# Performance work log

Measured on AMD Instinct MI355X. Metric: run time of the kernel, lower is better.

## Reference

```python
import jax, jax.numpy as jnp
import numpy as np

B, P, ED, AD, DD, E, V, T = 64, 196, 2048, 512, 512, 300, 1000, 96


def setup_inputs() -> dict:
    key = jax.random.key(0)
    ks = jax.random.split(key, 24)
    s = 0.02  # small init scale for weights
    lens = jax.random.randint(ks[2], (B,), 2, T + 1).astype(jnp.int32)
    lens = lens.at[0].set(T)  # ensure max(decode_lengths) == T-1 (static)
    return {
        'encoder_out': jax.random.normal(ks[0], (B, P, ED), jnp.float32),
        'encoded_captions': jax.random.randint(ks[1], (B, T), 0, V),
        'caption_lengths': lens,
        'emb': jax.random.uniform(ks[3], (V, E), jnp.float32, -0.1, 0.1),
        'W_enc_att': jax.random.normal(ks[4], (ED, AD), jnp.float32) * s,
        'b_enc_att': jnp.zeros((AD,), jnp.float32),
        'W_dec_att': jax.random.normal(ks[5], (DD, AD), jnp.float32) * s,
        'b_dec_att': jnp.zeros((AD,), jnp.float32),
        'w_full': jax.random.normal(ks[6], (AD,), jnp.float32) * s,
        'b_full': jnp.zeros((), jnp.float32),
        'W_init_h': jax.random.normal(ks[7], (ED, DD), jnp.float32) * s,
        'b_init_h': jnp.zeros((DD,), jnp.float32),
        'W_init_c': jax.random.normal(ks[8], (ED, DD), jnp.float32) * s,
        'b_init_c': jnp.zeros((DD,), jnp.float32),
        'W_fbeta': jax.random.normal(ks[9], (DD, ED), jnp.float32) * s,
        'b_fbeta': jnp.zeros((ED,), jnp.float32),
        'W_ih': jax.random.normal(ks[10], (E + ED, 4 * DD), jnp.float32) * s,
        'b_ih': jnp.zeros((4 * DD,), jnp.float32),
        'W_hh': jax.random.normal(ks[11], (DD, 4 * DD), jnp.float32) * s,
        'b_hh': jnp.zeros((4 * DD,), jnp.float32),
        'W_fc': jax.random.uniform(ks[12], (DD, V), jnp.float32, -0.1, 0.1),
        'b_fc': jnp.zeros((V,), jnp.float32),
    }


def reference(encoder_out, encoded_captions, caption_lengths, emb,
              W_enc_att, b_enc_att, W_dec_att, b_dec_att, w_full, b_full,
              W_init_h, b_init_h, W_init_c, b_init_c, W_fbeta, b_fbeta,
              W_ih, b_ih, W_hh, b_hh, W_fc, b_fc):
    # Sort by caption length, descending (stable like torch.sort on ints)
    sort_ind = jnp.argsort(-caption_lengths)
    lens = caption_lengths[sort_ind]
    eo = encoder_out[sort_ind]                  # [B,P,ED]
    caps = encoded_captions[sort_ind]           # [B,T]
    decode_lengths = lens - 1                   # [B]

    embs = emb[caps]                            # [B,T,E]
    mean_eo = eo.mean(axis=1)                   # [B,ED]
    h0 = mean_eo @ W_init_h + b_init_h          # [B,DD]
    c0 = mean_eo @ W_init_c + b_init_c

    # encoder-side attention projection is step-invariant: hoist it
    att1 = eo @ W_enc_att + b_enc_att           # [B,P,AD]

    Tdec = T - 1
    ts = jnp.arange(Tdec)
    masks = (decode_lengths[None, :] > ts[:, None]).astype(eo.dtype)  # [Tdec,B]
    emb_seq = jnp.swapaxes(embs[:, :Tdec, :], 0, 1)                    # [Tdec,B,E]

    def step(carry, xs):
        h, c = carry
        emb_t, m = xs                           # [B,E], [B]
        mb = m[:, None]
        # Bahdanau attention
        att2 = h @ W_dec_att + b_dec_att        # [B,AD]
        e = jnp.einsum('bpa,a->bp', jax.nn.relu(att1 + att2[:, None, :]), w_full) + b_full
        alpha = jax.nn.softmax(e, axis=1)       # [B,P]
        awe = jnp.einsum('bpd,bp->bd', eo, alpha)  # [B,ED]
        gate = jax.nn.sigmoid(h @ W_fbeta + b_fbeta)
        x = jnp.concatenate([emb_t, gate * awe], axis=1)  # [B,E+ED]
        # LSTMCell (torch gate order: i, f, g, o)
        gates = x @ W_ih + b_ih + h @ W_hh + b_hh
        i, f, g, o = jnp.split(gates, 4, axis=1)
        c_new = jax.nn.sigmoid(f) * c + jax.nn.sigmoid(i) * jnp.tanh(g)
        h_new = jax.nn.sigmoid(o) * jnp.tanh(c_new)
        # only active rows (sorted so they are a prefix) update state
        h2 = mb * h_new + (1.0 - mb) * h
        c2 = mb * c_new + (1.0 - mb) * c
        preds = (h2 @ W_fc + b_fc) * mb         # dropout = identity (eval)
        return (h2, c2), (preds, alpha * mb)

    (_, _), (preds, alphas) = jax.lax.scan(step, (h0, c0), (emb_seq, masks))
    predictions = jnp.swapaxes(preds, 0, 1)     # [B,Tdec,V]
    alphas = jnp.swapaxes(alphas, 0, 1)         # [B,Tdec,P]
    return predictions, caps, decode_lengths, alphas, sort_ind
```

## Files before the change

kernel.cpp:

```cpp
#include <hip/hip_runtime.h>
#include <stddef.h>
#include <math.h>

static constexpr int B = 64, P = 196, ED = 2048, AD = 512, DD = 512, E = 300, V = 1000, T = 96, TD = 95;
static constexpr int KX = E + ED;
static constexpr int KTOT = KX + DD;
static constexpr int KSPLIT = 8;
static constexpr int KPER = 368;
static constexpr int NG = 4 * DD;

static constexpr size_t POFF   = 0;
static constexpr size_t CAPOFF = (size_t)B * TD * V;
static constexpr size_t DLOFF  = CAPOFF + (size_t)B * T;
static constexpr size_t AOFF   = DLOFF + B;
static constexpr size_t SOFF   = AOFF + (size_t)B * TD * P;

__device__ __forceinline__ float sigm(float x) { return 1.0f / (1.0f + expf(-x)); }

__global__ __launch_bounds__(64) void k_sort(const int* __restrict__ lens,
                                             const int* __restrict__ caps_in,
                                             int* __restrict__ sidx,
                                             int* __restrict__ dlen,
                                             int* __restrict__ caps_s,
                                             float* __restrict__ out) {
    __shared__ int sl[B];
    __shared__ int ss[B];
    int i = threadIdx.x;
    sl[i] = lens[i];
    __syncthreads();
    int li = sl[i];
    int r = 0;
    for (int j = 0; j < B; j++) {
        int lj = sl[j];
        r += (lj > li) || (lj == li && j < i);
    }
    ss[r] = i;
    sidx[r] = i;
    dlen[r] = li - 1;
    out[DLOFF + r] = (float)(li - 1);
    out[SOFF + r] = (float)i;
    __syncthreads();
    for (int idx = i; idx < B * T; idx += B) {
        int b = idx / T, tt = idx % T;
        int v = caps_in[ss[b] * T + tt];
        caps_s[idx] = v;
        out[CAPOFF + idx] = (float)v;
    }
}

__global__ __launch_bounds__(256) void k_mean(const float* __restrict__ eo,
                                              const int* __restrict__ sidx,
                                              float* __restrict__ mean_eo) {
    int b = blockIdx.y;
    int d = blockIdx.x * 256 + threadIdx.x;
    const float* base = eo + ((size_t)sidx[b] * P) * ED + d;
    float s = 0.f;
    for (int p = 0; p < P; p++) s += base[(size_t)p * ED];
    mean_eo[(size_t)b * ED + d] = s * (1.0f / (float)P);
}

__global__ __launch_bounds__(256) void k_init(const float* __restrict__ mean_eo,
                                              const float* __restrict__ Wh, const float* __restrict__ bh,
                                              const float* __restrict__ Wc, const float* __restrict__ bc,
                                              float* __restrict__ h0, float* __restrict__ c0,
                                              float* __restrict__ xT) {
    int idx = blockIdx.x * 256 + threadIdx.x;
    int b = idx >> 9, j = idx & 511;
    const float* m = mean_eo + (size_t)b * ED;
    float ah = bh[j], ac = bc[j];
    for (int k = 0; k < ED; k++) {
        float mv = m[k];
        ah += mv * Wh[(size_t)k * DD + j];
        ac += mv * Wc[(size_t)k * DD + j];
    }
    h0[idx] = ah;
    c0[idx] = ac;
    xT[(size_t)(KX + j) * B + b] = ah;
}

__global__ __launch_bounds__(256) void k_att1(const float* __restrict__ eo,
                                              const float* __restrict__ W,
                                              const float* __restrict__ bias,
                                              const int* __restrict__ sidx,
                                              float* __restrict__ att1) {
    int m0 = blockIdx.x * 64, n0 = blockIdx.y * 64;
    __shared__ float sA[16][68];
    __shared__ float sB[16][68];
    int tid = threadIdx.x;
    int tx = tid & 15, ty = tid >> 4;
    float acc[4][4] = {};

    int la_m = tid >> 2;
    int la_k = (tid & 3) * 4;
    int lb_k = tid >> 4;
    int lb_n = (tid & 15) * 4;

    int mA = m0 + la_m;
    int bA = mA / P, pA = mA % P;
    const float* arow = eo + ((size_t)sidx[bA] * P + pA) * ED;

    for (int k0 = 0; k0 < ED; k0 += 16) {
        float4 av = *(const float4*)(arow + k0 + la_k);
        sA[la_k + 0][la_m] = av.x;
        sA[la_k + 1][la_m] = av.y;
        sA[la_k + 2][la_m] = av.z;
        sA[la_k + 3][la_m] = av.w;
        float4 bv = *(const float4*)(W + (size_t)(k0 + lb_k) * AD + n0 + lb_n);
        *(float4*)&sB[lb_k][lb_n] = bv;
        __syncthreads();
#pragma unroll
        for (int kk = 0; kk < 16; kk++) {
            float4 a4 = *(const float4*)&sA[kk][ty * 4];
            float4 b4 = *(const float4*)&sB[kk][tx * 4];
            float av_[4] = {a4.x, a4.y, a4.z, a4.w};
            float bv_[4] = {b4.x, b4.y, b4.z, b4.w};
#pragma unroll
            for (int i = 0; i < 4; i++)
#pragma unroll
                for (int j = 0; j < 4; j++) acc[i][j] += av_[i] * bv_[j];
        }
        __syncthreads();
    }
#pragma unroll
    for (int i = 0; i < 4; i++) {
        int m = m0 + ty * 4 + i;
        int n = n0 + tx * 4;
        float4 o;
        o.x = acc[i][0] + bias[n + 0];
        o.y = acc[i][1] + bias[n + 1];
        o.z = acc[i][2] + bias[n + 2];
        o.w = acc[i][3] + bias[n + 3];
        *(float4*)(att1 + (size_t)m * AD + n) = o;
    }
}

__global__ __launch_bounds__(256) void kA1(const float* __restrict__ hprev,
                                           const float* __restrict__ Wda, const float* __restrict__ bda,
                                           const float* __restrict__ Wfb, const float* __restrict__ bfb,
                                           const float* __restrict__ emb,
                                           const int* __restrict__ caps_s,
                                           float* __restrict__ att2g,
                                           float* __restrict__ fg,
                                           float* __restrict__ xT, int t) {
    int bx = blockIdx.x;
    int tid = threadIdx.x;
    if (bx >= 80) {
        int k0 = (bx - 80) * 60;
        for (int l = tid; l < 60 * 64; l += 256) {
            int r = l >> 6, b = l & 63;
            int k = k0 + r;
            int cap = caps_s[b * T + t];
            xT[(size_t)k * B + b] = emb[(size_t)cap * E + k];
        }
        return;
    }
    int n0 = bx * 32;
    bool is_att = (n0 < AD);
    __shared__ float sH[16][68];
    __shared__ float sW[16][36];
    float acc[4][2] = {};
    int tb = tid & 15, tn = tid >> 4;

    for (int k0 = 0; k0 < DD; k0 += 16) {
        {
            int b = tid >> 2, q = tid & 3;
            float4 hv = *(const float4*)(hprev + (size_t)b * DD + k0 + q * 4);
            sH[q * 4 + 0][b] = hv.x;
            sH[q * 4 + 1][b] = hv.y;
            sH[q * 4 + 2][b] = hv.z;
            sH[q * 4 + 3][b] = hv.w;
        }
        if (tid < 128) {
            int kk = tid >> 3, nn = (tid & 7) * 4;
            float4 wv;
            if (is_att) wv = *(const float4*)(Wda + (size_t)(k0 + kk) * AD + n0 + nn);
            else        wv = *(const float4*)(Wfb + (size_t)(k0 + kk) * ED + (n0 - AD) + nn);
            *(float4*)&sW[kk][nn] = wv;
        }
        __syncthreads();
#pragma unroll
        for (int kk = 0; kk < 16; kk++) {
            float4 hv = *(const float4*)&sH[kk][tb * 4];
            float w0 = sW[kk][tn * 2 + 0];
            float w1 = sW[kk][tn * 2 + 1];
            acc[0][0] += hv.x * w0; acc[0][1] += hv.x * w1;
            acc[1][0] += hv.y * w0; acc[1][1] += hv.y * w1;
            acc[2][0] += hv.z * w0; acc[2][1] += hv.z * w1;
            acc[3][0] += hv.w * w0; acc[3][1] += hv.w * w1;
        }
        __syncthreads();
    }
#pragma unroll
    for (int i = 0; i < 4; i++)
#pragma unroll
        for (int j = 0; j < 2; j++) {
            int b = tb * 4 + i;
            int n = n0 + tn * 2 + j;
            float v = acc[i][j];
            if (is_att) att2g[(size_t)b * AD + n] = v + bda[n];
            else {
                int d = n - AD;
                fg[(size_t)b * ED + d] = sigm(v + bfb[d]);
            }
        }
}

__global__ __launch_bounds__(256) void kA2(const float* __restrict__ att2g,
                                           const float* __restrict__ att1,
                                           const float* __restrict__ wf,
                                           const float* __restrict__ bfv,
                                           const int* __restrict__ dlen,
                                           float* __restrict__ alpha,
                                           float* __restrict__ out, int t) {
    int b = blockIdx.x;
    int tid = threadIdx.x;
    __shared__ float sa2[AD];
    __shared__ float swf[AD];
    __shared__ float se[P];
    __shared__ float red[256];

    sa2[tid] = att2g[(size_t)b * AD + tid];
    sa2[tid + 256] = att2g[(size_t)b * AD + tid + 256];
    swf[tid] = wf[tid];
    swf[tid + 256] = wf[tid + 256];
    __syncthreads();

    int w = tid >> 6, lane = tid & 63;
    float bf0 = bfv[0];
    for (int p = w; p < P; p += 4) {
        const float* row = att1 + ((size_t)b * P + p) * AD + lane * 8;
        float4 u0 = *(const float4*)row;
        float4 u1 = *(const float4*)(row + 4);
        float4 s0 = *(const float4*)&sa2[lane * 8];
        float4 s1 = *(const float4*)&sa2[lane * 8 + 4];
        float4 w0 = *(const float4*)&swf[lane * 8];
        float4 w1 = *(const float4*)&swf[lane * 8 + 4];
        float acc = fmaxf(u0.x + s0.x, 0.f) * w0.x + fmaxf(u0.y + s0.y, 0.f) * w0.y +
                    fmaxf(u0.z + s0.z, 0.f) * w0.z + fmaxf(u0.w + s0.w, 0.f) * w0.w +
                    fmaxf(u1.x + s1.x, 0.f) * w1.x + fmaxf(u1.y + s1.y, 0.f) * w1.y +
                    fmaxf(u1.z + s1.z, 0.f) * w1.z + fmaxf(u1.w + s1.w, 0.f) * w1.w;
#pragma unroll
        for (int m = 32; m >= 1; m >>= 1) acc += __shfl_xor(acc, m, 64);
        if (lane == 0) se[p] = acc + bf0;
    }
    __syncthreads();

    red[tid] = (tid < P) ? se[tid] : -1e30f;
    __syncthreads();
    for (int s = 128; s > 0; s >>= 1) {
        if (tid < s) red[tid] = fmaxf(red[tid], red[tid + s]);
        __syncthreads();
    }
    float mx = red[0];
    __syncthreads();
    float ex = (tid < P) ? expf(se[tid] - mx) : 0.f;
    red[tid] = ex;
    __syncthreads();
    for (int s = 128; s > 0; s >>= 1) {
        if (tid < s) red[tid] += red[tid + s];
        __syncthreads();
    }
    float inv = 1.0f / red[0];
    if (tid < P) {
        float a = ex * inv;
        alpha[(size_t)b * P + tid] = a;
        float m = (dlen[b] > t) ? 1.f : 0.f;
        out[AOFF + ((size_t)b * TD + t) * P + tid] = a * m;
    }
}

__global__ __launch_bounds__(256) void kB(const float* __restrict__ eo,
                                          const int* __restrict__ sidx,
                                          const float* __restrict__ alpha,
                                          const float* __restrict__ fg,
                                          float* __restrict__ xT) {
    int b = blockIdx.y, ch = blockIdx.x, tid = threadIdx.x;
    __shared__ float sal[P];
    if (tid < P) sal[tid] = alpha[(size_t)b * P + tid];
    __syncthreads();
    int d = ch * 256 + tid;
    const float* base = eo + ((size_t)sidx[b] * P) * ED + d;
    float aw = 0.f;
    for (int p = 0; p < P; p++) aw += base[(size_t)p * ED] * sal[p];
    xT[(size_t)(E + d) * B + b] = fg[(size_t)b * ED + d] * aw;
}

__global__ __launch_bounds__(256) void kC(const float* __restrict__ xT,
                                          const float* __restrict__ Wih,
                                          const float* __restrict__ Whh,
                                          float* __restrict__ part) {
    int bx = blockIdx.x;
    int ks = bx >> 6, nb = bx & 63;
    int n0 = nb * 32;
    int tid = threadIdx.x;
    int tb = tid & 15, tn = tid >> 4;
    __shared__ float sW[16][36];
    float acc[4][2] = {};
    int kbase = ks * KPER;

    for (int tile = 0; tile < 23; tile++) {
        int k0 = kbase + tile * 16;
        if (tid < 128) {
            int kk = tid >> 3, nn = (tid & 7) * 4;
            int kg = k0 + kk;
            float4 wv = make_float4(0.f, 0.f, 0.f, 0.f);
            if (kg < KX) wv = *(const float4*)&Wih[(size_t)kg * NG + n0 + nn];
            else if (kg < KTOT) wv = *(const float4*)&Whh[(size_t)(kg - KX) * NG + n0 + nn];
            *(float4*)&sW[kk][nn] = wv;
        }
        __syncthreads();
#pragma unroll
        for (int kk = 0; kk < 16; kk++) {
            int kg = k0 + kk;
            float4 xv = make_float4(0.f, 0.f, 0.f, 0.f);
            if (kg < KTOT) xv = *(const float4*)&xT[(size_t)kg * B + tb * 4];
            float w0 = sW[kk][tn * 2 + 0];
            float w1 = sW[kk][tn * 2 + 1];
            acc[0][0] += xv.x * w0; acc[0][1] += xv.x * w1;
            acc[1][0] += xv.y * w0; acc[1][1] += xv.y * w1;
            acc[2][0] += xv.z * w0; acc[2][1] += xv.z * w1;
            acc[3][0] += xv.w * w0; acc[3][1] += xv.w * w1;
        }
        __syncthreads();
    }
    float* pr = part + (size_t)ks * B * NG;
#pragma unroll
    for (int i = 0; i < 4; i++)
#pragma unroll
        for (int j = 0; j < 2; j++) {
            int b = tb * 4 + i, n = n0 + tn * 2 + j;
            pr[(size_t)b * NG + n] = acc[i][j];
        }
}

__global__ __launch_bounds__(256) void kD(const float* __restrict__ part,
                                          const float* __restrict__ bih,
                                          const float* __restrict__ bhh,
                                          const float* __restrict__ hprev,
                                          const float* __restrict__ cc,
                                          const int* __restrict__ dlen,
                                          float* __restrict__ hseq_t,
                                          float* __restrict__ cn,
                                          float* __restrict__ xT, int t) {
    int idx = blockIdx.x * 256 + threadIdx.x;
    int b = idx >> 9, j = idx & 511;
    float gi = bih[j] + bhh[j];
    float gf = bih[DD + j] + bhh[DD + j];
    float gg = bih[2 * DD + j] + bhh[2 * DD + j];
    float go = bih[3 * DD + j] + bhh[3 * DD + j];
#pragma unroll
    for (int s = 0; s < KSPLIT; s++) {
        const float* pr = part + ((size_t)s * B + b) * NG;
        gi += pr[j];
        gf += pr[DD + j];
        gg += pr[2 * DD + j];
        go += pr[3 * DD + j];
    }
    float cold = cc[idx], hold = hprev[idx];
    float cnew = sigm(gf) * cold + sigm(gi) * tanhf(gg);
    float hnew = sigm(go) * tanhf(cnew);
    bool m = dlen[b] > t;
    float h2 = m ? hnew : hold;
    float c2 = m ? cnew : cold;
    hseq_t[idx] = h2;
    cn[idx] = c2;
    xT[(size_t)(KX + j) * B + b] = h2;
}

__global__ __launch_bounds__(256) void k_predsall(const float* __restrict__ hseq,
                                                  const float* __restrict__ Wfc,
                                                  const float* __restrict__ bfc,
                                                  const int* __restrict__ dlen,
                                                  float* __restrict__ out) {
    int t = blockIdx.x;
    int n0 = blockIdx.y * 64;
    int tid = threadIdx.x;
    int tx = tid & 15, ty = tid >> 4;
    __shared__ float sA[16][68];
    __shared__ float sB[16][68];
    float acc[4][4] = {};
    const float* A = hseq + (size_t)t * B * DD;

    for (int k0 = 0; k0 < DD; k0 += 16) {
        {
            int b = tid >> 2, q = tid & 3;
            float4 hv = *(const float4*)(A + (size_t)b * DD + k0 + q * 4);
            sA[q * 4 + 0][b] = hv.x;
            sA[q * 4 + 1][b] = hv.y;
            sA[q * 4 + 2][b] = hv.z;
            sA[q * 4 + 3][b] = hv.w;
        }
        {
            int kk = tid >> 4, nn = (tid & 15) * 4;
            int c = n0 + nn;
            const float* wrow = Wfc + (size_t)(k0 + kk) * V;
            float4 wv;
            if (c + 3 < V) wv = *(const float4*)(wrow + c);
            else {
                wv.x = (c + 0 < V) ? wrow[c + 0] : 0.f;
                wv.y = (c + 1 < V) ? wrow[c + 1] : 0.f;
                wv.z = (c + 2 < V) ? wrow[c + 2] : 0.f;
                wv.w = (c + 3 < V) ? wrow[c + 3] : 0.f;
            }
            *(float4*)&sB[kk][nn] = wv;
        }
        __syncthreads();
#pragma unroll
        for (int kk = 0; kk < 16; kk++) {
            float4 a4 = *(const float4*)&sA[kk][ty * 4];
            float4 b4 = *(const float4*)&sB[kk][tx * 4];
            float av_[4] = {a4.x, a4.y, a4.z, a4.w};
            float bv_[4] = {b4.x, b4.y, b4.z, b4.w};
#pragma unroll
            for (int i = 0; i < 4; i++)
#pragma unroll
                for (int j = 0; j < 4; j++) acc[i][j] += av_[i] * bv_[j];
        }
        __syncthreads();
    }
#pragma unroll
    for (int i = 0; i < 4; i++) {
        int b = ty * 4 + i;
        bool m = dlen[b] > t;
#pragma unroll
        for (int j = 0; j < 4; j++) {
            int n = n0 + tx * 4 + j;
            if (n < V)
                out[POFF + ((size_t)b * TD + t) * V + n] = m ? (acc[i][j] + bfc[n]) : 0.f;
        }
    }
}

extern "C" void kernel_launch(void* const* d_in, const int* in_sizes, int n_in,
                              void* d_out, int out_size, void* d_ws, size_t ws_size,
                              hipStream_t stream) {
    const float* eo    = (const float*)d_in[0];
    const int*   caps  = (const int*)d_in[1];
    const int*   lens  = (const int*)d_in[2];
    const float* emb   = (const float*)d_in[3];
    const float* Wea   = (const float*)d_in[4];
    const float* bea   = (const float*)d_in[5];
    const float* Wda   = (const float*)d_in[6];
    const float* bda   = (const float*)d_in[7];
    const float* wfull = (const float*)d_in[8];
    const float* bfull = (const float*)d_in[9];
    const float* Wih_  = (const float*)d_in[10];
    const float* bih_  = (const float*)d_in[11];
    const float* Wic   = (const float*)d_in[12];
    const float* bic   = (const float*)d_in[13];
    const float* Wfb   = (const float*)d_in[14];
    const float* bfb   = (const float*)d_in[15];
    const float* Wih   = (const float*)d_in[16];
    const float* bih   = (const float*)d_in[17];
    const float* Whh   = (const float*)d_in[18];
    const float* bhh   = (const float*)d_in[19];
    const float* Wfc   = (const float*)d_in[20];
    const float* bfc   = (const float*)d_in[21];
    float* out = (float*)d_out;

    char* w = (char*)d_ws;
    auto carve = [&](size_t bytes) -> void* {
        void* p = (void*)w;
        w += (bytes + 255) & ~(size_t)255;
        return p;
    };
    int* sidx      = (int*)carve(B * 4);
    int* dlen      = (int*)carve(B * 4);
    int* caps_s    = (int*)carve((size_t)B * T * 4);
    float* mean_eo = (float*)carve((size_t)B * ED * 4);
    float* h0      = (float*)carve((size_t)B * DD * 4);
    float* cb0     = (float*)carve((size_t)B * DD * 4);
    float* cb1     = (float*)carve((size_t)B * DD * 4);
    float* att1    = (float*)carve((size_t)B * P * AD * 4);
    float* alphaW  = (float*)carve((size_t)B * P * 4);
    float* att2g   = (float*)carve((size_t)B * AD * 4);
    float* fg      = (float*)carve((size_t)B * ED * 4);
    float* xT      = (float*)carve((size_t)KTOT * B * 4);
    float* part    = (float*)carve((size_t)KSPLIT * B * NG * 4);
    float* hseq    = (float*)carve((size_t)TD * B * DD * 4);
    float* cb[2] = {cb0, cb1};

    k_sort<<<1, 64, 0, stream>>>(lens, caps, sidx, dlen, caps_s, out);
    k_mean<<<dim3(ED / 256, B), 256, 0, stream>>>(eo, sidx, mean_eo);
    k_init<<<(B * DD) / 256, 256, 0, stream>>>(mean_eo, Wih_, bih_, Wic, bic, h0, cb0, xT);
    k_att1<<<dim3((B * P) / 64, AD / 64), 256, 0, stream>>>(eo, Wea, bea, sidx, att1);

    for (int t = 0; t < TD; t++) {
        const float* hprev = (t == 0) ? h0 : (hseq + (size_t)(t - 1) * B * DD);
        float* cc = cb[t & 1];
        float* cn = cb[(t + 1) & 1];
        kA1<<<85, 256, 0, stream>>>(hprev, Wda, bda, Wfb, bfb, emb, caps_s, att2g, fg, xT, t);
        kA2<<<64, 256, 0, stream>>>(att2g, att1, wfull, bfull, dlen, alphaW, out, t);
        kB<<<dim3(8, B), 256, 0, stream>>>(eo, sidx, alphaW, fg, xT);
        kC<<<512, 256, 0, stream>>>(xT, Wih, Whh, part);
        kD<<<(B * DD) / 256, 256, 0, stream>>>(part, bih, bhh, hprev, cc, dlen,
                                               hseq + (size_t)t * B * DD, cn, xT, t);
    }
    k_predsall<<<dim3(TD, 16), 256, 0, stream>>>(hseq, Wfc, bfc, dlen, out);
}
```

Baseline: 19.51 ms.

## Fuse per-timestep decoder kernels into one persistent cooperative kernel with grid syncs

Replaces the five kernels launched per timestep with a single cooperative kernel (256 blocks of 512 threads) that loops over all timesteps and separates the phases with grid.sync(). This removes about 475 kernel launches and their gaps. The LSTM gate GEMM is also restructured: K-split is cut from 8 to 4, there is no shared-memory tiling, and each thread reads weights directly per column. In exchange, grid-wide barriers replace kernel boundaries, and the simpler GEMM may use bandwidth less efficiently.

```diff
diff --git a/kernel.cpp b/kernel.cpp
--- a/kernel.cpp
+++ b/kernel.cpp
@@ -1,12 +1,15 @@
 #include <hip/hip_runtime.h>
+#include <hip/hip_cooperative_groups.h>
 #include <stddef.h>
 #include <math.h>
+
+namespace cg = cooperative_groups;
 
 static constexpr int B = 64, P = 196, ED = 2048, AD = 512, DD = 512, E = 300, V = 1000, T = 96, TD = 95;
 static constexpr int KX = E + ED;
 static constexpr int KTOT = KX + DD;
-static constexpr int KSPLIT = 8;
-static constexpr int KPER = 368;
+static constexpr int NS = 4;
+static constexpr int KPER2 = KTOT / NS;
 static constexpr int NG = 4 * DD;
 
 static constexpr size_t POFF   = 0;
@@ -134,237 +137,209 @@
     }
 }
 
-__global__ __launch_bounds__(256) void kA1(const float* __restrict__ hprev,
-                                           const float* __restrict__ Wda, const float* __restrict__ bda,
-                                           const float* __restrict__ Wfb, const float* __restrict__ bfb,
-                                           const float* __restrict__ emb,
-                                           const int* __restrict__ caps_s,
-                                           float* __restrict__ att2g,
-                                           float* __restrict__ fg,
-                                           float* __restrict__ xT, int t) {
-    int bx = blockIdx.x;
-    int tid = threadIdx.x;
-    if (bx >= 80) {
-        int k0 = (bx - 80) * 60;
-        for (int l = tid; l < 60 * 64; l += 256) {
-            int r = l >> 6, b = l & 63;
-            int k = k0 + r;
-            int cap = caps_s[b * T + t];
-            xT[(size_t)k * B + b] = emb[(size_t)cap * E + k];
-        }
-        return;
-    }
-    int n0 = bx * 32;
-    bool is_att = (n0 < AD);
+__global__ __launch_bounds__(512, 2) void k_steps(
+    const float* __restrict__ eo, const int* __restrict__ sidx,
+    const int* __restrict__ dlen, const int* __restrict__ caps_s,
+    const float* __restrict__ emb,
+    const float* __restrict__ Wda, const float* __restrict__ bda,
+    const float* __restrict__ Wfb, const float* __restrict__ bfb,
+    const float* __restrict__ wfull, const float* __restrict__ bfull,
+    const float* __restrict__ att1,
+    const float* __restrict__ Wih, const float* __restrict__ Whh,
+    const float* __restrict__ bih, const float* __restrict__ bhh,
+    const float* __restrict__ h0, float* __restrict__ cb0, float* __restrict__ cb1,
+    float* __restrict__ att2g, float* __restrict__ fg, float* __restrict__ xT,
+    float* __restrict__ part, float* __restrict__ alphaW,
+    float* __restrict__ hseq, float* __restrict__ out)
+{
+    cg::grid_group grid = cg::this_grid();
+    const int bid = blockIdx.x;
+    const int tid = threadIdx.x;
+
     __shared__ float sH[16][68];
     __shared__ float sW[16][36];
-    float acc[4][2] = {};
-    int tb = tid & 15, tn = tid >> 4;
-
-    for (int k0 = 0; k0 < DD; k0 += 16) {
-        {
-            int b = tid >> 2, q = tid & 3;
-            float4 hv = *(const float4*)(hprev + (size_t)b * DD + k0 + q * 4);
-            sH[q * 4 + 0][b] = hv.x;
-            sH[q * 4 + 1][b] = hv.y;
-            sH[q * 4 + 2][b] = hv.z;
-            sH[q * 4 + 3][b] = hv.w;
-        }
-        if (tid < 128) {
-            int kk = tid >> 3, nn = (tid & 7) * 4;
-            float4 wv;
-            if (is_att) wv = *(const float4*)(Wda + (size_t)(k0 + kk) * AD + n0 + nn);
-            else        wv = *(const float4*)(Wfb + (size_t)(k0 + kk) * ED + (n0 - AD) + nn);
-            *(float4*)&sW[kk][nn] = wv;
-        }
-        __syncthreads();
-#pragma unroll
-        for (int kk = 0; kk < 16; kk++) {
-            float4 hv = *(const float4*)&sH[kk][tb * 4];
-            float w0 = sW[kk][tn * 2 + 0];
-            float w1 = sW[kk][tn * 2 + 1];
-            acc[0][0] += hv.x * w0; acc[0][1] += hv.x * w1;
-            acc[1][0] += hv.y * w0; acc[1][1] += hv.y * w1;
-            acc[2][0] += hv.z * w0; acc[2][1] += hv.z * w1;
-            acc[3][0] += hv.w * w0; acc[3][1] += hv.w * w1;
-        }
-        __syncthreads();
-    }
-#pragma unroll
-    for (int i = 0; i < 4; i++)
-#pragma unroll
-        for (int j = 0; j < 2; j++) {
-            int b = tb * 4 + i;
-            int n = n0 + tn * 2 + j;
-            float v = acc[i][j];
-            if (is_att) att2g[(size_t)b * AD + n] = v + bda[n];
-            else {
-                int d = n - AD;
-                fg[(size_t)b * ED + d] = sigm(v + bfb[d]);
-            }
-        }
-}
-
-__global__ __launch_bounds__(256) void kA2(const float* __restrict__ att2g,
-                                           const float* __restrict__ att1,
-                                           const float* __restrict__ wf,
-                                           const float* __restrict__ bfv,
-                                           const int* __restrict__ dlen,
-                                           float* __restrict__ alpha,
-                                           float* __restrict__ out, int t) {
-    int b = blockIdx.x;
-    int tid = threadIdx.x;
     __shared__ float sa2[AD];
     __shared__ float swf[AD];
     __shared__ float se[P];
-    __shared__ float red[256];
-
-    sa2[tid] = att2g[(size_t)b * AD + tid];
-    sa2[tid + 256] = att2g[(size_t)b * AD + tid + 256];
-    swf[tid] = wf[tid];
-    swf[tid + 256] = wf[tid + 256];
-    __syncthreads();
-
-    int w = tid >> 6, lane = tid & 63;
-    float bf0 = bfv[0];
-    for (int p = w; p < P; p += 4) {
-        const float* row = att1 + ((size_t)b * P + p) * AD + lane * 8;
-        float4 u0 = *(const float4*)row;
-        float4 u1 = *(const float4*)(row + 4);
-        float4 s0 = *(const float4*)&sa2[lane * 8];
-        float4 s1 = *(const float4*)&sa2[lane * 8 + 4];
-        float4 w0 = *(const float4*)&swf[lane * 8];
-        float4 w1 = *(const float4*)&swf[lane * 8 + 4];
-        float acc = fmaxf(u0.x + s0.x, 0.f) * w0.x + fmaxf(u0.y + s0.y, 0.f) * w0.y +
-                    fmaxf(u0.z + s0.z, 0.f) * w0.z + fmaxf(u0.w + s0.w, 0.f) * w0.w +
-                    fmaxf(u1.x + s1.x, 0.f) * w1.x + fmaxf(u1.y + s1.y, 0.f) * w1.y +
-                    fmaxf(u1.z + s1.z, 0.f) * w1.z + fmaxf(u1.w + s1.w, 0.f) * w1.w;
-#pragma unroll
-        for (int m = 32; m >= 1; m >>= 1) acc += __shfl_xor(acc, m, 64);
-        if (lane == 0) se[p] = acc + bf0;
-    }
-    __syncthreads();
-
-    red[tid] = (tid < P) ? se[tid] : -1e30f;
-    __syncthreads();
-    for (int s = 128; s > 0; s >>= 1) {
-        if (tid < s) red[tid] = fmaxf(red[tid], red[tid + s]);
-        __syncthreads();
-    }
-    float mx = red[0];
-    __syncthreads();
-    float ex = (tid < P) ? expf(se[tid] - mx) : 0.f;
-    red[tid] = ex;
-    __syncthreads();
-    for (int s = 128; s > 0; s >>= 1) {
-        if (tid < s) red[tid] += red[tid + s];
-        __syncthreads();
-    }
-    float inv = 1.0f / red[0];
-    if (tid < P) {
-        float a = ex * inv;
-        alpha[(size_t)b * P + tid] = a;
-        float m = (dlen[b] > t) ? 1.f : 0.f;
-        out[AOFF + ((size_t)b * TD + t) * P + tid] = a * m;
-    }
-}
-
-__global__ __launch_bounds__(256) void kB(const float* __restrict__ eo,
-                                          const int* __restrict__ sidx,
-                                          const float* __restrict__ alpha,
-                                          const float* __restrict__ fg,
-                                          float* __restrict__ xT) {
-    int b = blockIdx.y, ch = blockIdx.x, tid = threadIdx.x;
+    __shared__ float red[512];
     __shared__ float sal[P];
-    if (tid < P) sal[tid] = alpha[(size_t)b * P + tid];
-    __syncthreads();
-    int d = ch * 256 + tid;
-    const float* base = eo + ((size_t)sidx[b] * P) * ED + d;
-    float aw = 0.f;
-    for (int p = 0; p < P; p++) aw += base[(size_t)p * ED] * sal[p];
-    xT[(size_t)(E + d) * B + b] = fg[(size_t)b * ED + d] * aw;
-}
-
-__global__ __launch_bounds__(256) void kC(const float* __restrict__ xT,
-                                          const float* __restrict__ Wih,
-                                          const float* __restrict__ Whh,
-                                          float* __restrict__ part) {
-    int bx = blockIdx.x;
-    int ks = bx >> 6, nb = bx & 63;
-    int n0 = nb * 32;
-    int tid = threadIdx.x;
-    int tb = tid & 15, tn = tid >> 4;
-    __shared__ float sW[16][36];
-    float acc[4][2] = {};
-    int kbase = ks * KPER;
-
-    for (int tile = 0; tile < 23; tile++) {
-        int k0 = kbase + tile * 16;
-        if (tid < 128) {
-            int kk = tid >> 3, nn = (tid & 7) * 4;
-            int kg = k0 + kk;
-            float4 wv = make_float4(0.f, 0.f, 0.f, 0.f);
-            if (kg < KX) wv = *(const float4*)&Wih[(size_t)kg * NG + n0 + nn];
-            else if (kg < KTOT) wv = *(const float4*)&Whh[(size_t)(kg - KX) * NG + n0 + nn];
-            *(float4*)&sW[kk][nn] = wv;
-        }
-        __syncthreads();
-#pragma unroll
-        for (int kk = 0; kk < 16; kk++) {
-            int kg = k0 + kk;
-            float4 xv = make_float4(0.f, 0.f, 0.f, 0.f);
-            if (kg < KTOT) xv = *(const float4*)&xT[(size_t)kg * B + tb * 4];
-            float w0 = sW[kk][tn * 2 + 0];
-            float w1 = sW[kk][tn * 2 + 1];
-            acc[0][0] += xv.x * w0; acc[0][1] += xv.x * w1;
-            acc[1][0] += xv.y * w0; acc[1][1] += xv.y * w1;
-            acc[2][0] += xv.z * w0; acc[2][1] += xv.z * w1;
-            acc[3][0] += xv.w * w0; acc[3][1] += xv.w * w1;
-        }
-        __syncthreads();
-    }
-    float* pr = part + (size_t)ks * B * NG;
-#pragma unroll
-    for (int i = 0; i < 4; i++)
-#pragma unroll
-        for (int j = 0; j < 2; j++) {
-            int b = tb * 4 + i, n = n0 + tn * 2 + j;
-            pr[(size_t)b * NG + n] = acc[i][j];
-        }
-}
-
-__global__ __launch_bounds__(256) void kD(const float* __restrict__ part,
-                                          const float* __restrict__ bih,
-                                          const float* __restrict__ bhh,
-                                          const float* __restrict__ hprev,
-                                          const float* __restrict__ cc,
-                                          const int* __restrict__ dlen,
-                                          float* __restrict__ hseq_t,
-                                          float* __restrict__ cn,
-                                          float* __restrict__ xT, int t) {
-    int idx = blockIdx.x * 256 + threadIdx.x;
-    int b = idx >> 9, j = idx & 511;
-    float gi = bih[j] + bhh[j];
-    float gf = bih[DD + j] + bhh[DD + j];
-    float gg = bih[2 * DD + j] + bhh[2 * DD + j];
-    float go = bih[3 * DD + j] + bhh[3 * DD + j];
-#pragma unroll
-    for (int s = 0; s < KSPLIT; s++) {
-        const float* pr = part + ((size_t)s * B + b) * NG;
-        gi += pr[j];
-        gf += pr[DD + j];
-        gg += pr[2 * DD + j];
-        go += pr[3 * DD + j];
-    }
-    float cold = cc[idx], hold = hprev[idx];
-    float cnew = sigm(gf) * cold + sigm(gi) * tanhf(gg);
-    float hnew = sigm(go) * tanhf(cnew);
-    bool m = dlen[b] > t;
-    float h2 = m ? hnew : hold;
-    float c2 = m ? cnew : cold;
-    hseq_t[idx] = h2;
-    cn[idx] = c2;
-    xT[(size_t)(KX + j) * B + b] = h2;
+
+#pragma unroll 1
+    for (int t = 0; t < TD; t++) {
+        const float* hprev = (t == 0) ? h0 : (hseq + (size_t)(t - 1) * B * DD);
+
+        if (bid < 80) {
+            int n0 = bid * 32;
+            bool is_att = (n0 < AD);
+            const float* W = is_att ? Wda : Wfb;
+            int ld = is_att ? AD : ED;
+            int colb = is_att ? n0 : (n0 - AD);
+            int tb = tid & 15, tn = tid >> 4;
+            float a0 = 0.f, a1 = 0.f, a2 = 0.f, a3 = 0.f;
+            for (int k0 = 0; k0 < DD; k0 += 16) {
+                if (tid < 256) {
+                    int b = tid >> 2, q = tid & 3;
+                    float4 hv = *(const float4*)(hprev + (size_t)b * DD + k0 + q * 4);
+                    sH[q * 4 + 0][b] = hv.x;
+                    sH[q * 4 + 1][b] = hv.y;
+                    sH[q * 4 + 2][b] = hv.z;
+                    sH[q * 4 + 3][b] = hv.w;
+                }
+                if (tid < 128) {
+                    int kk = tid >> 3, nn = (tid & 7) * 4;
+                    *(float4*)&sW[kk][nn] = *(const float4*)(W + (size_t)(k0 + kk) * ld + colb + nn);
+                }
+                __syncthreads();
+#pragma unroll
+                for (int kk = 0; kk < 16; kk++) {
+                    float4 hv = *(const float4*)&sH[kk][tb * 4];
+                    float wv = sW[kk][tn];
+                    a0 += hv.x * wv; a1 += hv.y * wv; a2 += hv.z * wv; a3 += hv.w * wv;
+                }
+                __syncthreads();
+            }
+            float accv[4] = {a0, a1, a2, a3};
+            int n = n0 + tn;
+            if (is_att) {
+                float bv = bda[n];
+#pragma unroll
+                for (int i = 0; i < 4; i++)
+                    att2g[(size_t)(tb * 4 + i) * AD + n] = accv[i] + bv;
+            } else {
+                int d = n - AD;
+                float bv = bfb[d];
+#pragma unroll
+                for (int i = 0; i < 4; i++)
+                    fg[(size_t)(tb * 4 + i) * ED + d] = sigm(accv[i] + bv);
+            }
+        } else if (bid < 85) {
+            int k0 = (bid - 80) * 60;
+            for (int l = tid; l < 60 * 64; l += 512) {
+                int r = l >> 6, b = l & 63;
+                int k = k0 + r;
+                int cap = caps_s[b * T + t];
+                xT[(size_t)k * B + b] = emb[(size_t)cap * E + k];
+            }
+        }
+        grid.sync();
+
+        if (bid < B) {
+            int b = bid;
+            sa2[tid] = att2g[(size_t)b * AD + tid];
+            swf[tid] = wfull[tid];
+            __syncthreads();
+            int wv_ = tid >> 6, lane = tid & 63;
+            float bf0 = bfull[0];
+            for (int p = wv_; p < P; p += 8) {
+                const float* row = att1 + ((size_t)b * P + p) * AD + lane * 8;
+                float4 u0 = *(const float4*)row;
+                float4 u1 = *(const float4*)(row + 4);
+                float4 s0 = *(const float4*)&sa2[lane * 8];
+                float4 s1 = *(const float4*)&sa2[lane * 8 + 4];
+                float4 w0 = *(const float4*)&swf[lane * 8];
+                float4 w1 = *(const float4*)&swf[lane * 8 + 4];
+                float acc = fmaxf(u0.x + s0.x, 0.f) * w0.x + fmaxf(u0.y + s0.y, 0.f) * w0.y +
+                            fmaxf(u0.z + s0.z, 0.f) * w0.z + fmaxf(u0.w + s0.w, 0.f) * w0.w +
+                            fmaxf(u1.x + s1.x, 0.f) * w1.x + fmaxf(u1.y + s1.y, 0.f) * w1.y +
+                            fmaxf(u1.z + s1.z, 0.f) * w1.z + fmaxf(u1.w + s1.w, 0.f) * w1.w;
+#pragma unroll
+                for (int mm = 32; mm >= 1; mm >>= 1) acc += __shfl_xor(acc, mm, 64);
+                if (lane == 0) se[p] = acc + bf0;
+            }
+            __syncthreads();
+            red[tid] = (tid < P) ? se[tid] : -1e30f;
+            __syncthreads();
+            for (int s = 256; s > 0; s >>= 1) {
+                if (tid < s) red[tid] = fmaxf(red[tid], red[tid + s]);
+                __syncthreads();
+            }
+            float mx = red[0];
+            __syncthreads();
+            float ex = (tid < P) ? expf(se[tid] - mx) : 0.f;
+            red[tid] = ex;
+            __syncthreads();
+            for (int s = 256; s > 0; s >>= 1) {
+                if (tid < s) red[tid] += red[tid + s];
+                __syncthreads();
+            }
+            float inv = 1.0f / red[0];
+            if (tid < P) {
+                float a = ex * inv;
+                alphaW[(size_t)b * P + tid] = a;
+                float m = (dlen[b] > t) ? 1.f : 0.f;
+                out[AOFF + ((size_t)b * TD + t) * P + tid] = a * m;
+            }
+        }
+        grid.sync();
+
+        {
+            int b = bid >> 2, ch = bid & 3;
+            if (tid < P) sal[tid] = alphaW[(size_t)b * P + tid];
+            __syncthreads();
+            int d = ch * 512 + tid;
+            const float* base = eo + ((size_t)sidx[b] * P) * ED + d;
+            float aw = 0.f;
+#pragma unroll 4
+            for (int p = 0; p < P; p++) aw += base[(size_t)p * ED] * sal[p];
+            xT[(size_t)(E + d) * B + b] = fg[(size_t)b * ED + d] * aw;
+            __syncthreads();
+        }
+        grid.sync();
+
+        {
+            int ks = bid & 3, nt = bid >> 2;
+            int n0 = nt * 32;
+            int tb = tid & 15, tn = tid >> 4;
+            int n = n0 + tn;
+            float a0 = 0.f, a1 = 0.f, a2 = 0.f, a3 = 0.f;
+            int klo = ks * KPER2, khi = klo + KPER2;
+            int kmid = (khi < KX) ? khi : KX;
+            for (int k = klo; k < kmid; k++) {
+                float4 xv = *(const float4*)&xT[(size_t)k * B + tb * 4];
+                float wv = Wih[(size_t)k * NG + n];
+                a0 += xv.x * wv; a1 += xv.y * wv; a2 += xv.z * wv; a3 += xv.w * wv;
+            }
+            for (int k = (klo > KX ? klo : KX); k < khi; k++) {
+                float4 xv = *(const float4*)&xT[(size_t)k * B + tb * 4];
+                float wv = Whh[(size_t)(k - KX) * NG + n];
+                a0 += xv.x * wv; a1 += xv.y * wv; a2 += xv.z * wv; a3 += xv.w * wv;
+            }
+            float* pr = part + (size_t)ks * B * NG + n;
+            pr[(size_t)(tb * 4 + 0) * NG] = a0;
+            pr[(size_t)(tb * 4 + 1) * NG] = a1;
+            pr[(size_t)(tb * 4 + 2) * NG] = a2;
+            pr[(size_t)(tb * 4 + 3) * NG] = a3;
+        }
+        grid.sync();
+
+        if (bid < B) {
+            int b = bid, j = tid;
+            const float* cc = (t & 1) ? cb1 : cb0;
+            float* cn = (t & 1) ? cb0 : cb1;
+            float gi = bih[j] + bhh[j];
+            float gf = bih[DD + j] + bhh[DD + j];
+            float gg = bih[2 * DD + j] + bhh[2 * DD + j];
+            float go = bih[3 * DD + j] + bhh[3 * DD + j];
+#pragma unroll
+            for (int s = 0; s < NS; s++) {
+                const float* pr = part + ((size_t)s * B + b) * NG;
+                gi += pr[j];
+                gf += pr[DD + j];
+                gg += pr[2 * DD + j];
+                go += pr[3 * DD + j];
+            }
+            float cold = cc[(size_t)b * DD + j], hold = hprev[(size_t)b * DD + j];
+            float cnew = sigm(gf) * cold + sigm(gi) * tanhf(gg);
+            float hnew = sigm(go) * tanhf(cnew);
+            bool m = dlen[b] > t;
+            float h2 = m ? hnew : hold;
+            float c2 = m ? cnew : cold;
+            hseq[(size_t)t * B * DD + (size_t)b * DD + j] = h2;
+            cn[(size_t)b * DD + j] = c2;
+            xT[(size_t)(KX + j) * B + b] = h2;
+        }
+        grid.sync();
+    }
 }
 
 __global__ __launch_bounds__(256) void k_predsall(const float* __restrict__ hseq,
@@ -476,25 +451,24 @@
     float* att2g   = (float*)carve((size_t)B * AD * 4);
     float* fg      = (float*)carve((size_t)B * ED * 4);
     float* xT      = (float*)carve((size_t)KTOT * B * 4);
-    float* part    = (float*)carve((size_t)KSPLIT * B * NG * 4);
+    float* part    = (float*)carve((size_t)NS * B * NG * 4);
     float* hseq    = (float*)carve((size_t)TD * B * DD * 4);
-    float* cb[2] = {cb0, cb1};
 
     k_sort<<<1, 64, 0, stream>>>(lens, caps, sidx, dlen, caps_s, out);
     k_mean<<<dim3(ED / 256, B), 256, 0, stream>>>(eo, sidx, mean_eo);
     k_init<<<(B * DD) / 256, 256, 0, stream>>>(mean_eo, Wih_, bih_, Wic, bic, h0, cb0, xT);
     k_att1<<<dim3((B * P) / 64, AD / 64), 256, 0, stream>>>(eo, Wea, bea, sidx, att1);
 
-    for (int t = 0; t < TD; t++) {
-        const float* hprev = (t == 0) ? h0 : (hseq + (size_t)(t - 1) * B * DD);
-        float* cc = cb[t & 1];
-        float* cn = cb[(t + 1) & 1];
-        kA1<<<85, 256, 0, stream>>>(hprev, Wda, bda, Wfb, bfb, emb, caps_s, att2g, fg, xT, t);
-        kA2<<<64, 256, 0, stream>>>(att2g, att1, wfull, bfull, dlen, alphaW, out, t);
-        kB<<<dim3(8, B), 256, 0, stream>>>(eo, sidx, alphaW, fg, xT);
-        kC<<<512, 256, 0, stream>>>(xT, Wih, Whh, part);
-        kD<<<(B * DD) / 256, 256, 0, stream>>>(part, bih, bhh, hprev, cc, dlen,
-                                               hseq + (size_t)t * B * DD, cn, xT, t);
-    }
+    void* kargs[] = {
+        (void*)&eo, (void*)&sidx, (void*)&dlen, (void*)&caps_s, (void*)&emb,
+        (void*)&Wda, (void*)&bda, (void*)&Wfb, (void*)&bfb,
+        (void*)&wfull, (void*)&bfull, (void*)&att1,
+        (void*)&Wih, (void*)&Whh, (void*)&bih, (void*)&bhh,
+        (void*)&h0, (void*)&cb0, (void*)&cb1,
+        (void*)&att2g, (void*)&fg, (void*)&xT, (void*)&part, (void*)&alphaW,
+        (void*)&hseq, (void*)&out
+    };
+    hipLaunchCooperativeKernel((void*)k_steps, dim3(256), dim3(512), kargs, 0, stream);
+
     k_predsall<<<dim3(TD, 16), 256, 0, stream>>>(hseq, Wfc, bfc, dlen, out);
 }
```

New measurement: 38.89 ms. 1.99x slower.

## Fuse attention softmax with context sum and LSTM gemm with cell update

Applied to the files above, without the earlier changes.

Cuts the per-step launches from five to three. The attention scores, softmax and weighted encoder sum now run in one 1024-thread kernel, split four ways per batch row. The LSTM split-K gemm and the cell update are merged: the last-arriving block per column group, found through an atomic counter, reduces the partials and applies the gates, with gate columns regrouped so each block covers matching i/f/g/o slices. Embedding gathers are precomputed for all steps, and the h state is double-buffered in xT to avoid read/write hazards. In exchange it adds atomic synchronisation, redundant softmax work in each of the four chunks, and a memory-ordering risk on the partial sums.

```diff
diff --git a/kernel.cpp b/kernel.cpp
--- a/kernel.cpp
+++ b/kernel.cpp
@@ -22,11 +22,13 @@
                                              int* __restrict__ sidx,
                                              int* __restrict__ dlen,
                                              int* __restrict__ caps_s,
+                                             unsigned int* __restrict__ cnt,
                                              float* __restrict__ out) {
     __shared__ int sl[B];
     __shared__ int ss[B];
     int i = threadIdx.x;
     sl[i] = lens[i];
+    cnt[i] = 0u;
     __syncthreads();
     int li = sl[i];
     int r = 0;
@@ -45,6 +47,19 @@
         int v = caps_in[ss[b] * T + tt];
         caps_s[idx] = v;
         out[CAPOFF + idx] = (float)v;
+    }
+}
+
+__global__ __launch_bounds__(256) void k_emball(const float* __restrict__ emb,
+                                                const int* __restrict__ caps_s,
+                                                float* __restrict__ embT) {
+    int t = blockIdx.x;
+    int k0 = blockIdx.y * 60;
+    for (int l = threadIdx.x; l < 60 * 64; l += 256) {
+        int r = l >> 6, b = l & 63;
+        int k = k0 + r;
+        int cap = caps_s[b * T + t];
+        embT[((size_t)t * E + k) * B + b] = emb[(size_t)cap * E + k];
     }
 }
 
@@ -75,7 +90,7 @@
     }
     h0[idx] = ah;
     c0[idx] = ac;
-    xT[(size_t)(KX + j) * B + b] = ah;
+    xT[(size_t)(KX + DD + j) * B + b] = ah;
 }
 
 __global__ __launch_bounds__(256) void k_att1(const float* __restrict__ eo,
@@ -134,31 +149,18 @@
     }
 }
 
-__global__ __launch_bounds__(256) void kA1(const float* __restrict__ hprev,
-                                           const float* __restrict__ Wda, const float* __restrict__ bda,
-                                           const float* __restrict__ Wfb, const float* __restrict__ bfb,
-                                           const float* __restrict__ emb,
-                                           const int* __restrict__ caps_s,
-                                           float* __restrict__ att2g,
-                                           float* __restrict__ fg,
-                                           float* __restrict__ xT, int t) {
+__global__ __launch_bounds__(256) void kA1w(const float* __restrict__ hprev,
+                                            const float* __restrict__ Wda, const float* __restrict__ bda,
+                                            const float* __restrict__ Wfb, const float* __restrict__ bfb,
+                                            float* __restrict__ att2g,
+                                            float* __restrict__ fg) {
     int bx = blockIdx.x;
     int tid = threadIdx.x;
-    if (bx >= 80) {
-        int k0 = (bx - 80) * 60;
-        for (int l = tid; l < 60 * 64; l += 256) {
-            int r = l >> 6, b = l & 63;
-            int k = k0 + r;
-            int cap = caps_s[b * T + t];
-            xT[(size_t)k * B + b] = emb[(size_t)cap * E + k];
-        }
-        return;
-    }
-    int n0 = bx * 32;
-    bool is_att = (n0 < AD);
+    bool is_att = (bx < 32);
+    int n0 = is_att ? bx * 16 : (bx - 32) * 16;
     __shared__ float sH[16][68];
-    __shared__ float sW[16][36];
-    float acc[4][2] = {};
+    __shared__ float sW[16][20];
+    float acc[4] = {};
     int tb = tid & 15, tn = tid >> 4;
 
     for (int k0 = 0; k0 < DD; k0 += 16) {
@@ -170,64 +172,60 @@
             sH[q * 4 + 2][b] = hv.z;
             sH[q * 4 + 3][b] = hv.w;
         }
-        if (tid < 128) {
-            int kk = tid >> 3, nn = (tid & 7) * 4;
+        if (tid < 64) {
+            int kk = tid >> 2, nn = (tid & 3) * 4;
             float4 wv;
             if (is_att) wv = *(const float4*)(Wda + (size_t)(k0 + kk) * AD + n0 + nn);
-            else        wv = *(const float4*)(Wfb + (size_t)(k0 + kk) * ED + (n0 - AD) + nn);
+            else        wv = *(const float4*)(Wfb + (size_t)(k0 + kk) * ED + n0 + nn);
             *(float4*)&sW[kk][nn] = wv;
         }
         __syncthreads();
 #pragma unroll
         for (int kk = 0; kk < 16; kk++) {
             float4 hv = *(const float4*)&sH[kk][tb * 4];
-            float w0 = sW[kk][tn * 2 + 0];
-            float w1 = sW[kk][tn * 2 + 1];
-            acc[0][0] += hv.x * w0; acc[0][1] += hv.x * w1;
-            acc[1][0] += hv.y * w0; acc[1][1] += hv.y * w1;
-            acc[2][0] += hv.z * w0; acc[2][1] += hv.z * w1;
-            acc[3][0] += hv.w * w0; acc[3][1] += hv.w * w1;
-        }
-        __syncthreads();
-    }
-#pragma unroll
-    for (int i = 0; i < 4; i++)
-#pragma unroll
-        for (int j = 0; j < 2; j++) {
-            int b = tb * 4 + i;
-            int n = n0 + tn * 2 + j;
-            float v = acc[i][j];
-            if (is_att) att2g[(size_t)b * AD + n] = v + bda[n];
-            else {
-                int d = n - AD;
-                fg[(size_t)b * ED + d] = sigm(v + bfb[d]);
-            }
-        }
-}
-
-__global__ __launch_bounds__(256) void kA2(const float* __restrict__ att2g,
-                                           const float* __restrict__ att1,
-                                           const float* __restrict__ wf,
-                                           const float* __restrict__ bfv,
-                                           const int* __restrict__ dlen,
-                                           float* __restrict__ alpha,
-                                           float* __restrict__ out, int t) {
-    int b = blockIdx.x;
+            float wv = sW[kk][tn];
+            acc[0] += hv.x * wv;
+            acc[1] += hv.y * wv;
+            acc[2] += hv.z * wv;
+            acc[3] += hv.w * wv;
+        }
+        __syncthreads();
+    }
+    int n = n0 + tn;
+#pragma unroll
+    for (int i = 0; i < 4; i++) {
+        int b = tb * 4 + i;
+        if (is_att) att2g[(size_t)b * AD + n] = acc[i] + bda[n];
+        else        fg[(size_t)b * ED + n] = sigm(acc[i] + bfb[n]);
+    }
+}
+
+__global__ __launch_bounds__(1024) void kA2B(const float* __restrict__ att2g,
+                                             const float* __restrict__ att1,
+                                             const float* __restrict__ wf,
+                                             const float* __restrict__ bfv,
+                                             const int* __restrict__ dlen,
+                                             const float* __restrict__ eo,
+                                             const int* __restrict__ sidx,
+                                             const float* __restrict__ fg,
+                                             float* __restrict__ xT,
+                                             float* __restrict__ out, int t) {
+    int bid = blockIdx.x;
+    int b = bid >> 2, ch = bid & 3;
     int tid = threadIdx.x;
     __shared__ float sa2[AD];
     __shared__ float swf[AD];
     __shared__ float se[P];
-    __shared__ float red[256];
-
-    sa2[tid] = att2g[(size_t)b * AD + tid];
-    sa2[tid + 256] = att2g[(size_t)b * AD + tid + 256];
-    swf[tid] = wf[tid];
-    swf[tid + 256] = wf[tid + 256];
+    __shared__ float red[1024];
+    __shared__ float partl[8][512];
+
+    if (tid < 512) sa2[tid] = att2g[(size_t)b * AD + tid];
+    else           swf[tid - 512] = wf[tid - 512];
     __syncthreads();
 
     int w = tid >> 6, lane = tid & 63;
     float bf0 = bfv[0];
-    for (int p = w; p < P; p += 4) {
+    for (int p = w; p < P; p += 16) {
         const float* row = att1 + ((size_t)b * P + p) * AD + lane * 8;
         float4 u0 = *(const float4*)row;
         float4 u1 = *(const float4*)(row + 4);
@@ -240,14 +238,14 @@
                     fmaxf(u1.x + s1.x, 0.f) * w1.x + fmaxf(u1.y + s1.y, 0.f) * w1.y +
                     fmaxf(u1.z + s1.z, 0.f) * w1.z + fmaxf(u1.w + s1.w, 0.f) * w1.w;
 #pragma unroll
-        for (int m = 32; m >= 1; m >>= 1) acc += __shfl_xor(acc, m, 64);
+        for (int mm = 32; mm >= 1; mm >>= 1) acc += __shfl_xor(acc, mm, 64);
         if (lane == 0) se[p] = acc + bf0;
     }
     __syncthreads();
 
     red[tid] = (tid < P) ? se[tid] : -1e30f;
     __syncthreads();
-    for (int s = 128; s > 0; s >>= 1) {
+    for (int s = 512; s > 0; s >>= 1) {
         if (tid < s) red[tid] = fmaxf(red[tid], red[tid + s]);
         __syncthreads();
     }
@@ -256,64 +254,88 @@
     float ex = (tid < P) ? expf(se[tid] - mx) : 0.f;
     red[tid] = ex;
     __syncthreads();
-    for (int s = 128; s > 0; s >>= 1) {
+    for (int s = 512; s > 0; s >>= 1) {
         if (tid < s) red[tid] += red[tid + s];
         __syncthreads();
     }
     float inv = 1.0f / red[0];
+    __syncthreads();
     if (tid < P) {
         float a = ex * inv;
-        alpha[(size_t)b * P + tid] = a;
-        float m = (dlen[b] > t) ? 1.f : 0.f;
-        out[AOFF + ((size_t)b * TD + t) * P + tid] = a * m;
-    }
-}
-
-__global__ __launch_bounds__(256) void kB(const float* __restrict__ eo,
-                                          const int* __restrict__ sidx,
-                                          const float* __restrict__ alpha,
-                                          const float* __restrict__ fg,
-                                          float* __restrict__ xT) {
-    int b = blockIdx.y, ch = blockIdx.x, tid = threadIdx.x;
-    __shared__ float sal[P];
-    if (tid < P) sal[tid] = alpha[(size_t)b * P + tid];
-    __syncthreads();
-    int d = ch * 256 + tid;
+        se[tid] = a;
+        if (ch == 0) {
+            float m = (dlen[b] > t) ? 1.f : 0.f;
+            out[AOFF + ((size_t)b * TD + t) * P + tid] = a * m;
+        }
+    }
+    __syncthreads();
+
+    int pg = tid >> 7, q = tid & 127;
+    int d = ch * 512 + q * 4;
     const float* base = eo + ((size_t)sidx[b] * P) * ED + d;
-    float aw = 0.f;
-    for (int p = 0; p < P; p++) aw += base[(size_t)p * ED] * sal[p];
-    xT[(size_t)(E + d) * B + b] = fg[(size_t)b * ED + d] * aw;
-}
-
-__global__ __launch_bounds__(256) void kC(const float* __restrict__ xT,
-                                          const float* __restrict__ Wih,
-                                          const float* __restrict__ Whh,
-                                          float* __restrict__ part) {
+    float ax = 0.f, ay = 0.f, az = 0.f, aw = 0.f;
+    for (int p = pg; p < P; p += 8) {
+        float4 v = *(const float4*)(base + (size_t)p * ED);
+        float a = se[p];
+        ax += v.x * a; ay += v.y * a; az += v.z * a; aw += v.w * a;
+    }
+    partl[pg][q * 4 + 0] = ax;
+    partl[pg][q * 4 + 1] = ay;
+    partl[pg][q * 4 + 2] = az;
+    partl[pg][q * 4 + 3] = aw;
+    __syncthreads();
+    if (tid < 512) {
+        float s = partl[0][tid] + partl[1][tid] + partl[2][tid] + partl[3][tid] +
+                  partl[4][tid] + partl[5][tid] + partl[6][tid] + partl[7][tid];
+        int d2 = ch * 512 + tid;
+        xT[(size_t)(E + d2) * B + b] = fg[(size_t)b * ED + d2] * s;
+    }
+}
+
+__global__ __launch_bounds__(256) void kCD(const float* __restrict__ xT,
+                                           const float* __restrict__ embT_t,
+                                           const float* __restrict__ xh_r,
+                                           const float* __restrict__ Wih,
+                                           const float* __restrict__ Whh,
+                                           float* __restrict__ part,
+                                           unsigned int* __restrict__ cnt,
+                                           const float* __restrict__ bih,
+                                           const float* __restrict__ bhh,
+                                           const float* __restrict__ h0,
+                                           float* __restrict__ hseq,
+                                           const float* __restrict__ cread,
+                                           float* __restrict__ cwrite,
+                                           const int* __restrict__ dlen,
+                                           float* __restrict__ xh_w, int t) {
     int bx = blockIdx.x;
     int ks = bx >> 6, nb = bx & 63;
-    int n0 = nb * 32;
     int tid = threadIdx.x;
     int tb = tid & 15, tn = tid >> 4;
     __shared__ float sW[16][36];
+    __shared__ unsigned int sOld;
     float acc[4][2] = {};
     int kbase = ks * KPER;
 
     for (int tile = 0; tile < 23; tile++) {
         int k0 = kbase + tile * 16;
         if (tid < 128) {
-            int kk = tid >> 3, nn = (tid & 7) * 4;
+            int kk = tid >> 3, seg = tid & 7;
+            int g = seg >> 1, half = seg & 1;
             int kg = k0 + kk;
+            int col = g * 512 + nb * 8 + half * 4;
             float4 wv = make_float4(0.f, 0.f, 0.f, 0.f);
-            if (kg < KX) wv = *(const float4*)&Wih[(size_t)kg * NG + n0 + nn];
-            else if (kg < KTOT) wv = *(const float4*)&Whh[(size_t)(kg - KX) * NG + n0 + nn];
-            *(float4*)&sW[kk][nn] = wv;
+            if (kg < KX) wv = *(const float4*)&Wih[(size_t)kg * NG + col];
+            else if (kg < KTOT) wv = *(const float4*)&Whh[(size_t)(kg - KX) * NG + col];
+            *(float4*)&sW[kk][seg * 4] = wv;
         }
         __syncthreads();
 #pragma unroll
         for (int kk = 0; kk < 16; kk++) {
             int kg = k0 + kk;
             float4 xv = make_float4(0.f, 0.f, 0.f, 0.f);
-            if (kg < KTOT) xv = *(const float4*)&xT[(size_t)kg * B + tb * 4];
+            if (kg < E) xv = *(const float4*)&embT_t[(size_t)kg * B + tb * 4];
+            else if (kg < KX) xv = *(const float4*)&xT[(size_t)kg * B + tb * 4];
+            else if (kg < KTOT) xv = *(const float4*)&xh_r[(size_t)(kg - KX) * B + tb * 4];
             float w0 = sW[kk][tn * 2 + 0];
             float w1 = sW[kk][tn * 2 + 1];
             acc[0][0] += xv.x * w0; acc[0][1] += xv.x * w1;
@@ -323,48 +345,50 @@
         }
         __syncthreads();
     }
-    float* pr = part + (size_t)ks * B * NG;
 #pragma unroll
     for (int i = 0; i < 4; i++)
 #pragma unroll
         for (int j = 0; j < 2; j++) {
-            int b = tb * 4 + i, n = n0 + tn * 2 + j;
-            pr[(size_t)b * NG + n] = acc[i][j];
-        }
-}
-
-__global__ __launch_bounds__(256) void kD(const float* __restrict__ part,
-                                          const float* __restrict__ bih,
-                                          const float* __restrict__ bhh,
-                                          const float* __restrict__ hprev,
-                                          const float* __restrict__ cc,
-                                          const int* __restrict__ dlen,
-                                          float* __restrict__ hseq_t,
-                                          float* __restrict__ cn,
-                                          float* __restrict__ xT, int t) {
-    int idx = blockIdx.x * 256 + threadIdx.x;
-    int b = idx >> 9, j = idx & 511;
-    float gi = bih[j] + bhh[j];
-    float gf = bih[DD + j] + bhh[DD + j];
-    float gg = bih[2 * DD + j] + bhh[2 * DD + j];
-    float go = bih[3 * DD + j] + bhh[3 * DD + j];
-#pragma unroll
-    for (int s = 0; s < KSPLIT; s++) {
-        const float* pr = part + ((size_t)s * B + b) * NG;
-        gi += pr[j];
-        gf += pr[DD + j];
-        gg += pr[2 * DD + j];
-        go += pr[3 * DD + j];
-    }
-    float cold = cc[idx], hold = hprev[idx];
-    float cnew = sigm(gf) * cold + sigm(gi) * tanhf(gg);
-    float hnew = sigm(go) * tanhf(cnew);
-    bool m = dlen[b] > t;
-    float h2 = m ? hnew : hold;
-    float c2 = m ? cnew : cold;
-    hseq_t[idx] = h2;
-    cn[idx] = c2;
-    xT[(size_t)(KX + j) * B + b] = h2;
+            int b = tb * 4 + i, lc = tn * 2 + j;
+            __hip_atomic_store(&part[((size_t)ks * B + b) * NG + nb * 32 + lc], acc[i][j],
+                               __ATOMIC_RELAXED, __HIP_MEMORY_SCOPE_AGENT);
+        }
+    __syncthreads();
+    if (tid == 0)
+        sOld = __hip_atomic_fetch_add(&cnt[nb], 1u, __ATOMIC_ACQ_REL, __HIP_MEMORY_SCOPE_AGENT);
+    __syncthreads();
+    if (sOld != 7u) return;
+
+    if (tid == 0)
+        __hip_atomic_store(&cnt[nb], 0u, __ATOMIC_RELAXED, __HIP_MEMORY_SCOPE_AGENT);
+
+    const float* holds = (t == 0) ? h0 : (hseq + (size_t)(t - 1) * B * DD);
+#pragma unroll
+    for (int rep = 0; rep < 2; rep++) {
+        int idx = rep * 256 + tid;
+        int bb = idx & 63, jj = idx >> 6;
+        int j = nb * 8 + jj;
+        float g4[4];
+#pragma unroll
+        for (int g = 0; g < 4; g++) {
+            float gv = bih[g * DD + j] + bhh[g * DD + j];
+#pragma unroll
+            for (int s = 0; s < KSPLIT; s++)
+                gv += __hip_atomic_load(&part[((size_t)s * B + bb) * NG + nb * 32 + g * 8 + jj],
+                                        __ATOMIC_RELAXED, __HIP_MEMORY_SCOPE_AGENT);
+            g4[g] = gv;
+        }
+        float cold = cread[(size_t)bb * DD + j];
+        float hold = holds[(size_t)bb * DD + j];
+        float cnew = sigm(g4[1]) * cold + sigm(g4[0]) * tanhf(g4[2]);
+        float hnew = sigm(g4[3]) * tanhf(cnew);
+        bool m = dlen[bb] > t;
+        float h2 = m ? hnew : hold;
+        float c2 = m ? cnew : cold;
+        hseq[(size_t)t * B * DD + (size_t)bb * DD + j] = h2;
+        cwrite[(size_t)bb * DD + j] = c2;
+        xh_w[(size_t)j * B + bb] = h2;
+    }
 }
 
 __global__ __launch_bounds__(256) void k_predsall(const float* __restrict__ hseq,
@@ -467,34 +491,34 @@
     int* sidx      = (int*)carve(B * 4);
     int* dlen      = (int*)carve(B * 4);
     int* caps_s    = (int*)carve((size_t)B * T * 4);
+    unsigned int* cnt = (unsigned int*)carve(64 * 4);
     float* mean_eo = (float*)carve((size_t)B * ED * 4);
     float* h0      = (float*)carve((size_t)B * DD * 4);
     float* cb0     = (float*)carve((size_t)B * DD * 4);
     float* cb1     = (float*)carve((size_t)B * DD * 4);
     float* att1    = (float*)carve((size_t)B * P * AD * 4);
-    float* alphaW  = (float*)carve((size_t)B * P * 4);
     float* att2g   = (float*)carve((size_t)B * AD * 4);
     float* fg      = (float*)carve((size_t)B * ED * 4);
-    float* xT      = (float*)carve((size_t)KTOT * B * 4);
+    float* xT      = (float*)carve((size_t)(KTOT + DD) * B * 4);
     float* part    = (float*)carve((size_t)KSPLIT * B * NG * 4);
     float* hseq    = (float*)carve((size_t)TD * B * DD * 4);
+    float* embT    = (float*)carve((size_t)TD * E * B * 4);
     float* cb[2] = {cb0, cb1};
 
-    k_sort<<<1, 64, 0, stream>>>(lens, caps, sidx, dlen, caps_s, out);
+    k_sort<<<1, 64, 0, stream>>>(lens, caps, sidx, dlen, caps_s, cnt, out);
+    k_emball<<<dim3(TD, 5), 256, 0, stream>>>(emb, caps_s, embT);
     k_mean<<<dim3(ED / 256, B), 256, 0, stream>>>(eo, sidx, mean_eo);
-    k_init<<<(B * DD) / 256, 256, 0, stream>>>(mean_eo, Wih_, bih_, Wic, bic, h0, cb0, xT);
+    k_init<<<(B * DD) / 256, 256, 0, stream>>>(mean_eo, Wih_, bih_, Wic, bic, h0, cb1, xT);
     k_att1<<<dim3((B * P) / 64, AD / 64), 256, 0, stream>>>(eo, Wea, bea, sidx, att1);
 
     for (int t = 0; t < TD; t++) {
         const float* hprev = (t == 0) ? h0 : (hseq + (size_t)(t - 1) * B * DD);
-        float* cc = cb[t & 1];
-        float* cn = cb[(t + 1) & 1];
-        kA1<<<85, 256, 0, stream>>>(hprev, Wda, bda, Wfb, bfb, emb, caps_s, att2g, fg, xT, t);
-        kA2<<<64, 256, 0, stream>>>(att2g, att1, wfull, bfull, dlen, alphaW, out, t);
-        kB<<<dim3(8, B), 256, 0, stream>>>(eo, sidx, alphaW, fg, xT);
-        kC<<<512, 256, 0, stream>>>(xT, Wih, Whh, part);
-        kD<<<(B * DD) / 256, 256, 0, stream>>>(part, bih, bhh, hprev, cc, dlen,
-                                               hseq + (size_t)t * B * DD, cn, xT, t);
+        kA1w<<<160, 256, 0, stream>>>(hprev, Wda, bda, Wfb, bfb, att2g, fg);
+        kA2B<<<256, 1024, 0, stream>>>(att2g, att1, wfull, bfull, dlen, eo, sidx, fg, xT, out, t);
+        const float* xh_r = xT + (size_t)(KX + ((t + 1) & 1) * DD) * B;
+        float*       xh_w = xT + (size_t)(KX + (t & 1) * DD) * B;
+        kCD<<<512, 256, 0, stream>>>(xT, embT + (size_t)t * E * B, xh_r, Wih, Whh, part, cnt,
+                                     bih, bhh, h0, hseq, cb[(t + 1) & 1], cb[t & 1], dlen, xh_w, t);
     }
     k_predsall<<<dim3(TD, 16), 256, 0, stream>>>(hseq, Wfc, bfc, dlen, out);
 }
```

After: 19.01 ms. 1.03x faster.
